# Kernel optimization log

Measured on AMD Instinct MI355X. Metric: run time of the kernel, lower is better.

## Reference

```python
import jax, jax.numpy as jnp
import numpy as np

N_LOC = 20000
N_EXP = 200000
H = 64
E = 1500000
L = 400000


def setup_inputs() -> dict:
    key = jax.random.key(0)
    ks = jax.random.split(key, 24)
    f = jnp.float32
    w = lambda k, shp: jax.random.normal(k, shp, dtype=f) * 0.1
    # edges: ('location','of','experts'): src in [0,N_LOC), dst in [0,N_EXP)
    src = jax.random.randint(ks[0], (E,), 0, N_LOC)
    dst = jax.random.randint(ks[1], (E,), 0, N_EXP)
    edge_of = jnp.stack([src, dst])          # location -> experts
    edge_rev = jnp.stack([dst, src])         # experts -> location (ToUndirected)
    row = jax.random.randint(ks[2], (L,), 0, N_LOC)
    col = jax.random.randint(ks[3], (L,), 0, N_EXP)
    edge_label_index = jnp.stack([row, col])
    return dict(
        emb_loc=w(ks[4], (N_LOC, H)), emb_exp=w(ks[5], (N_EXP, H)),
        W1l_of=w(ks[6], (H, H)), b1_of=jnp.zeros((H,), f), W1r_of=w(ks[7], (H, H)),
        W1l_rev=w(ks[8], (H, H)), b1_rev=jnp.zeros((H,), f), W1r_rev=w(ks[9], (H, H)),
        W2l_of=w(ks[10], (H, H)), b2_of=jnp.zeros((H,), f), W2r_of=w(ks[11], (H, H)),
        W2l_rev=w(ks[12], (H, H)), b2_rev=jnp.zeros((H,), f), W2r_rev=w(ks[13], (H, H)),
        dW1=w(ks[14], (2 * H, H)), db1=jnp.zeros((H,), f),
        dW2=w(ks[15], (H, 1)), db2=jnp.zeros((1,), f),
        edge_of=edge_of, edge_rev=edge_rev, edge_label_index=edge_label_index,
    )


def _sage(x_src, x_dst, edge, Wl, b, Wr, n_dst):
    # PyG SAGEConv: lin_l(mean of neighbor msgs) + lin_r(x_dst); bias only in lin_l
    s, d = edge[0], edge[1]
    msg = x_src[s]                                   # [E, H] gather
    summed = jax.ops.segment_sum(msg, d, num_segments=n_dst)
    cnt = jax.ops.segment_sum(jnp.ones((edge.shape[1],), x_src.dtype), d, num_segments=n_dst)
    agg = summed / jnp.maximum(cnt, 1.0)[:, None]
    return agg @ Wl + b + x_dst @ Wr


def reference(emb_loc, emb_exp,
              W1l_of, b1_of, W1r_of, W1l_rev, b1_rev, W1r_rev,
              W2l_of, b2_of, W2r_of, W2l_rev, b2_rev, W2r_rev,
              dW1, db1, dW2, db2,
              edge_of, edge_rev, edge_label_index):
    # layer 1 (to_hetero: one conv per edge type; each dst type has one incoming type)
    z_exp = jax.nn.relu(_sage(emb_loc, emb_exp, edge_of, W1l_of, b1_of, W1r_of, N_EXP))
    z_loc = jax.nn.relu(_sage(emb_exp, emb_loc, edge_rev, W1l_rev, b1_rev, W1r_rev, N_LOC))
    # layer 2 (no relu)
    z_exp2 = _sage(z_loc, z_exp, edge_of, W2l_of, b2_of, W2r_of, N_EXP)
    z_loc2 = _sage(z_exp, z_loc, edge_rev, W2l_rev, b2_rev, W2r_rev, N_LOC)
    # EdgeDecoder: gather-concat-MLP
    row, col = edge_label_index[0], edge_label_index[1]
    z = jnp.concatenate([z_loc2[row], z_exp2[col]], axis=-1)  # [L, 2H]
    h = jax.nn.relu(z @ dW1 + db1)
    out = (h @ dW2 + db2).reshape(-1)
    return out
```

## Files before the change

kernel.cpp:

```cpp
#include <hip/hip_runtime.h>

#define H 64
#define NE 1500000
#define NLOC 20000
#define NEXP 200000
#define NL 400000
#define PAD_E 32
#define PAD_L 128

#define EB 896
#define NBE 224
#define LB 112
#define NBL 179
#define BIN_CHUNK 2048
#define NBIN ((NE + BIN_CHUNK - 1) / BIN_CHUNK)
#define EBSLOT 28
#define LBSLOT 32
#define ECAP 8192
#define LCAP 10240
#define FCAP 4096

#define WS_NEED 90546112ULL

typedef int vint4 __attribute__((ext_vector_type(4)));
typedef _Float16 f16x8 __attribute__((ext_vector_type(8)));
typedef _Float16 f16x4 __attribute__((ext_vector_type(4)));
typedef float f32x4 __attribute__((ext_vector_type(4)));
typedef unsigned int u32;
typedef unsigned short u16;
typedef unsigned long long u64;

__device__ __forceinline__ float bcastf(float v, int k) {
  return __int_as_float(__builtin_amdgcn_readlane(__float_as_int(v), k));
}
__device__ __forceinline__ int bcasti(int v, int k) {
  return __builtin_amdgcn_readlane(v, k);
}
__device__ __forceinline__ int sel4(int g, int n0, int n1, int n2, int n3) {
  return (g & 2) ? ((g & 1) ? n3 : n2) : ((g & 1) ? n1 : n0);
}

__global__ __launch_bounds__(256) void bin_kernel(
    const int* __restrict__ src, const int* __restrict__ dst,
    u32* __restrict__ expQ, u32* __restrict__ locQ,
    int* __restrict__ qcnt, int* __restrict__ flbk_cnt,
    u64* __restrict__ flbkQ)
{
  __shared__ u32 eb[NBE * EBSLOT];
  __shared__ u32 lb[NBL * LBSLOT];
  __shared__ int ec[NBE], lc[NBL], ebase[NBE], lbase[NBL];

  const int tid = threadIdx.x;
  for (int i = tid; i < NBE; i += 256) ec[i] = 0;
  for (int i = tid; i < NBL; i += 256) lc[i] = 0;
  __syncthreads();

  const long base = (long)blockIdx.x * BIN_CHUNK + tid * 8;
  if (base < NE) {
    vint4 s0 = __builtin_nontemporal_load((const vint4*)(src + base));
    vint4 s1 = __builtin_nontemporal_load((const vint4*)(src + base + 4));
    vint4 d0 = __builtin_nontemporal_load((const vint4*)(dst + base));
    vint4 d1 = __builtin_nontemporal_load((const vint4*)(dst + base + 4));
    int ss[8] = {s0.x, s0.y, s0.z, s0.w, s1.x, s1.y, s1.z, s1.w};
    int dd[8] = {d0.x, d0.y, d0.z, d0.w, d1.x, d1.y, d1.z, d1.w};
#pragma unroll
    for (int k = 0; k < 8; k++) {
      const u32 d = (u32)dd[k], s = (u32)ss[k];
      {
        const u32 b = d / (u32)EB;
        const int pos = atomicAdd(&ec[b], 1);
        if (pos < EBSLOT) {
          eb[b * EBSLOT + pos] = ((d - b * EB) << 16) | s;
        } else {
          int fi = atomicAdd(flbk_cnt, 1);
          if (fi < FCAP) flbkQ[fi] = ((u64)d << 32) | (u64)s;
        }
      }
      {
        const u32 b = s / (u32)LB;
        const int pos = atomicAdd(&lc[b], 1);
        if (pos < LBSLOT) {
          lb[b * LBSLOT + pos] = ((s - b * LB) << 18) | d;
        } else {
          int fi = atomicAdd(flbk_cnt, 1);
          if (fi < FCAP) flbkQ[fi] = (1ULL << 63) | ((u64)s << 32) | (u64)d;
        }
      }
    }
  }
  __syncthreads();

  for (int i = tid; i < NBE; i += 256) {
    const int c = min(ec[i], EBSLOT);
    ebase[i] = c ? atomicAdd(&qcnt[i], c) : 0;
  }
  for (int i = tid; i < NBL; i += 256) {
    const int c = min(lc[i], LBSLOT);
    lbase[i] = c ? atomicAdd(&qcnt[NBE + i], c) : 0;
  }
  __syncthreads();

  const int wid = tid >> 6, ln = tid & 63;
  for (int b = wid; b < NBE; b += 4) {
    const int c = min(ec[b], EBSLOT);
    if (ln < c) {
      const int idx = ebase[b] + ln;
      const u32 r = eb[b * EBSLOT + ln];
      if (idx < ECAP) {
        expQ[(long)b * ECAP + idx] = r;
      } else {
        int fi = atomicAdd(flbk_cnt, 1);
        if (fi < FCAP)
          flbkQ[fi] = ((u64)(b * EB + (r >> 16)) << 32) | (u64)(r & 0xFFFF);
      }
    }
  }
  for (int b = wid; b < NBL; b += 4) {
    const int c = min(lc[b], LBSLOT);
    if (ln < c) {
      const int idx = lbase[b] + ln;
      const u32 r = lb[b * LBSLOT + ln];
      if (idx < LCAP) {
        locQ[(long)b * LCAP + idx] = r;
      } else {
        int fi = atomicAdd(flbk_cnt, 1);
        if (fi < FCAP)
          flbkQ[fi] = (1ULL << 63) | ((u64)(b * LB + (r >> 18)) << 32) |
                      (u64)(r & 0x3FFFF);
      }
    }
  }
}

__global__ __launch_bounds__(256) void build_kernel(
    const u32* __restrict__ expQ, const u32* __restrict__ locQ,
    const int* __restrict__ qcnt,
    u16* __restrict__ nbr_exp, int* __restrict__ nbr_loc,
    int* __restrict__ cnt_exp, int* __restrict__ cnt_loc)
{
  __shared__ char ldsraw[60928];
  const int tid = threadIdx.x;
  if (blockIdx.x < NBE) {
    const int b = blockIdx.x;
    u16* rows = (u16*)ldsraw;
    int* cnts = (int*)(ldsraw + 57344);
    for (int i = tid; i < EB; i += 256) cnts[i] = 0;
    __syncthreads();
    const int n = min(qcnt[b], ECAP);
    for (int i = tid; i < n; i += 256) {
      const u32 r = expQ[(long)b * ECAP + i];
      const int nl = (int)(r >> 16);
      const int pos = atomicAdd(&cnts[nl], 1);
      if (pos < PAD_E) rows[nl * PAD_E + pos] = (u16)(r & 0xFFFF);
    }
    __syncthreads();
    const int node0 = b * EB;
    const int nn = min(EB, NEXP - node0);
    u32* grows = (u32*)(nbr_exp + (long)node0 * PAD_E);
    const u32* lrows = (const u32*)rows;
    for (int j = tid; j < nn * (PAD_E / 2); j += 256) grows[j] = lrows[j];
    for (int i = tid; i < nn; i += 256) cnt_exp[node0 + i] = cnts[i];
  } else {
    const int b = blockIdx.x - NBE;
    int* rows = (int*)ldsraw;
    int* cnts = (int*)(ldsraw + 57344);
    for (int i = tid; i < LB; i += 256) cnts[i] = 0;
    __syncthreads();
    const int n = min(qcnt[NBE + b], LCAP);
    for (int i = tid; i < n; i += 256) {
      const u32 r = locQ[(long)b * LCAP + i];
      const int sl = (int)(r >> 18);
      const int pos = atomicAdd(&cnts[sl], 1);
      if (pos < PAD_L) rows[sl * PAD_L + pos] = (int)(r & 0x3FFFF);
    }
    __syncthreads();
    const int node0 = b * LB;
    const int nn = min(LB, NLOC - node0);
    int* grows = nbr_loc + (long)node0 * PAD_L;
    for (int j = tid; j < nn * PAD_L; j += 256) grows[j] = rows[j];
    for (int i = tid; i < nn; i += 256) cnt_loc[node0 + i] = cnts[i];
  }
}

__global__ __launch_bounds__(256) void prep_kernel(
    const float* __restrict__ W2r_of, const float* __restrict__ W2l_of,
    const float* __restrict__ W2l_rev, const float* __restrict__ W2r_rev,
    const float* __restrict__ dW1, const float* __restrict__ b2_of,
    const float* __restrict__ b2_rev,
    float* __restrict__ Wf_q, float* __restrict__ Wf_y2,
    float* __restrict__ Wf_t2, float* __restrict__ Wf_p,
    float* __restrict__ bf_q, float* __restrict__ bf_p,
    const int* __restrict__ flbk_cnt, const u64* __restrict__ flbkQ,
    u16* __restrict__ nbr_exp, int* __restrict__ nbr_loc,
    int* __restrict__ cnt_exp, int* __restrict__ cnt_loc,
    const float* __restrict__ emb_loc, _Float16* __restrict__ Ylh,
    const float* __restrict__ W1l_of,
    const float* __restrict__ W1r_of, const float* __restrict__ W1l_rev,
    const float* __restrict__ W1r_rev,
    _Float16* __restrict__ W1rT16, _Float16* __restrict__ W1lrT16,
    _Float16* __restrict__ WfqT16,
    _Float16* __restrict__ W1rRevH16, _Float16* __restrict__ Wt2H16,
    _Float16* __restrict__ WpH16)
{
  const int lane = threadIdx.x & 63;
  const int w = threadIdx.x >> 6;
  const float* dW1a = dW1;
  const float* dW1b = dW1 + H * H;
  if (blockIdx.x < 4) {
    const float* A; const float* B; float* C;
    _Float16* CT; _Float16* CH;
    switch (blockIdx.x) {
      case 0:  A = W2r_of;  B = dW1b; C = Wf_q;  CT = WfqT16; CH = nullptr; break;
      case 1:  A = W2l_of;  B = dW1b; C = Wf_y2; CT = nullptr; CH = nullptr; break;
      case 2:  A = W2l_rev; B = dW1a; C = Wf_t2; CT = nullptr; CH = Wt2H16; break;
      default: A = W2r_rev; B = dW1a; C = Wf_p;  CT = nullptr; CH = WpH16;  break;
    }
    float b[H];
#pragma unroll
    for (int k = 0; k < H; k++) b[k] = B[k * H + lane];
    for (int r = w * 16; r < w * 16 + 16; r++) {
      const float xv = A[r * H + lane];
      float a0 = 0.f, a1 = 0.f;
#pragma unroll
      for (int k = 0; k < H; k += 2) {
        a0 += bcastf(xv, k)     * b[k];
        a1 += bcastf(xv, k + 1) * b[k + 1];
      }
      const float val = a0 + a1;
      C[r * H + lane] = val;
      if (CT) CT[(long)lane * H + r] = (_Float16)val;
      if (CH) CH[(long)r * H + lane] = (_Float16)val;
    }
  } else if (blockIdx.x == 4) {
    if (w < 2) {
      const float* bv_src = (w == 0) ? b2_of : b2_rev;
      const float* B      = (w == 0) ? dW1b  : dW1a;
      float* o            = (w == 0) ? bf_q  : bf_p;
      float wk[H];
#pragma unroll
      for (int k = 0; k < H; k++) wk[k] = B[k * H + lane];
      const float bv = bv_src[lane];
      float a = 0.f;
#pragma unroll
      for (int k = 0; k < H; k++) a += bcastf(bv, k) * wk[k];
      o[lane] = a;
    }
  } else if (blockIdx.x == 5) {
    const int n = min(*flbk_cnt, FCAP);
    for (int i = threadIdx.x; i < n; i += 256) {
      const u64 rec = flbkQ[i];
      const int node = (int)((rec >> 32) & 0x3FFFF);
      const int val  = (int)(rec & 0x3FFFF);
      if ((rec >> 63) == 0) {
        int pos = atomicAdd(&cnt_exp[node], 1);
        if (pos < PAD_E) nbr_exp[(long)node * PAD_E + pos] = (u16)val;
      } else {
        int pos = atomicAdd(&cnt_loc[node], 1);
        if (pos < PAD_L) nbr_loc[(long)node * PAD_L + pos] = val;
      }
    }
  } else if (blockIdx.x < 8) {
    const float* S = (blockIdx.x == 6) ? W1r_of : W1l_rev;
    _Float16* D    = (blockIdx.x == 6) ? W1rT16 : W1lrT16;
    for (int k = w * 16; k < w * 16 + 16; k++)
      D[(long)lane * H + k] = (_Float16)S[(long)k * H + lane];
  } else if (blockIdx.x == 8) {
    for (int k = w * 16; k < w * 16 + 16; k++)
      W1rRevH16[(long)k * H + lane] = (_Float16)W1r_rev[(long)k * H + lane];
  } else {
    float wreg[H];
#pragma unroll
    for (int k = 0; k < H; k++) wreg[k] = W1l_of[k * H + lane];
    const int gw2 = (blockIdx.x - 9) * 4 + w;
    for (int r = gw2; r < NLOC; r += 5000) {
      const float xv = emb_loc[(long)r * H + lane];
      float a0 = 0.f, a1 = 0.f;
#pragma unroll
      for (int k = 0; k < H; k += 2) {
        a0 += bcastf(xv, k)     * wreg[k];
        a1 += bcastf(xv, k + 1) * wreg[k + 1];
      }
      Ylh[(long)r * H + lane] = (_Float16)(a0 + a1);
    }
  }
}

__global__ __launch_bounds__(256, 4) void dense_linear_kernel(
    const float* __restrict__ x, _Float16* __restrict__ out16,
    const float* __restrict__ W, int n)
{
  const int lane = threadIdx.x & 63;
  const int gw = (blockIdx.x * 256 + threadIdx.x) >> 6;
  const int nw = (gridDim.x * 256) >> 6;
  float w[H];
#pragma unroll
  for (int k = 0; k < H; k++) w[k] = W[k * H + lane];
  for (int i = gw; i < n; i += nw) {
    const float xv = x[i * H + lane];
    float a0 = 0.f, a1 = 0.f;
#pragma unroll
    for (int k = 0; k < H; k += 2) {
      a0 += bcastf(xv, k)     * w[k];
      a1 += bcastf(xv, k + 1) * w[k + 1];
    }
    out16[i * H + lane] = (_Float16)(a0 + a1);
  }
}

__global__ __launch_bounds__(256, 4) void mfma_pass_kernel(
    const u16* __restrict__ nbr, const int* __restrict__ cnt,
    const _Float16* __restrict__ y,
    const float* a32, const _Float16* a16,
    _Float16* out1, const _Float16* __restrict__ W1T,
    const float* __restrict__ bias, int relu,
    _Float16* out2, const _Float16* __restrict__ W2T)
{
  const int w = threadIdx.x >> 6;
  const int lane = threadIdx.x & 63;
  const int q = lane >> 4;
  const int cidx = lane & 15;
  const int rb = blockIdx.x * 16;

  __shared__ float Gs[16 * 68];

  const _Float16* bt1 = W1T + (long)(w * 16 + cidx) * H;
  f16x8 b1lo = *(const f16x8*)(bt1 + q * 8);
  f16x8 b1hi = *(const f16x8*)(bt1 + 32 + q * 8);
  f16x8 b2lo, b2hi;
  if (out2) {
    const _Float16* bt2 = W2T + (long)(w * 16 + cidx) * H;
    b2lo = *(const f16x8*)(bt2 + q * 8);
    b2hi = *(const f16x8*)(bt2 + 32 + q * 8);
  }

  f16x8 a0, a1;
  if (a16) {
    const _Float16* ar = a16 + (long)(rb + cidx) * H;
    a0 = *(const f16x8*)(ar + q * 8);
    a1 = *(const f16x8*)(ar + 32 + q * 8);
  } else {
    const float* ar = a32 + (long)(rb + cidx) * H;
    f32x4 v0 = *(const f32x4*)(ar + q * 8);
    f32x4 v1 = *(const f32x4*)(ar + q * 8 + 4);
    f32x4 v2 = *(const f32x4*)(ar + 32 + q * 8);
    f32x4 v3 = *(const f32x4*)(ar + 32 + q * 8 + 4);
#pragma unroll
    for (int j = 0; j < 4; j++) {
      a0[j] = (_Float16)v0[j];
      a0[j + 4] = (_Float16)v1[j];
      a1[j] = (_Float16)v2[j];
      a1[j + 4] = (_Float16)v3[j];
    }
  }

  if (y) {
    const int i0r = rb + w * 4;
    const int g = lane >> 4;
    const int sub = lane & 15;
    int c4v[4];
#pragma unroll
    for (int rr = 0; rr < 4; rr++) c4v[rr] = cnt[i0r + rr];
    int id4[4];
#pragma unroll
    for (int rr = 0; rr < 4; rr++) {
      const int c = min(c4v[rr], PAD_E);
      id4[rr] = (lane < c) ? (int)nbr[(long)(i0r + rr) * PAD_E + lane] : 0;
    }
#pragma unroll
    for (int rr = 0; rr < 4; rr++) {
      const int cc = min(c4v[rr], PAD_E);
      const int id = id4[rr];
      const int kl = cc - 1;
      float s0 = 0.f, s1 = 0.f, s2 = 0.f, s3 = 0.f;
      for (int k = 0; k < cc; k += 4) {
        const int n0 = bcasti(id, k);
        const int n1 = bcasti(id, min(k + 1, kl));
        const int n2 = bcasti(id, min(k + 2, kl));
        const int n3 = bcasti(id, min(k + 3, kl));
        const int ns = sel4(g, n0, n1, n2, n3);
        const f16x4 v = *(const f16x4*)(y + (long)ns * H + sub * 4);
        const float msk = (k + g < cc) ? 1.0f : 0.0f;
        s0 = fmaf(msk, (float)v[0], s0);
        s1 = fmaf(msk, (float)v[1], s1);
        s2 = fmaf(msk, (float)v[2], s2);
        s3 = fmaf(msk, (float)v[3], s3);
      }
      s0 += __shfl_xor(s0, 16); s0 += __shfl_xor(s0, 32);
      s1 += __shfl_xor(s1, 16); s1 += __shfl_xor(s1, 32);
      s2 += __shfl_xor(s2, 16); s2 += __shfl_xor(s2, 32);
      s3 += __shfl_xor(s3, 16); s3 += __shfl_xor(s3, 32);
      const float inv = 1.0f / fmaxf((float)c4v[rr], 1.0f);
      if (lane < 16) {
        float* gp = &Gs[(w * 4 + rr) * 68 + 4 * lane];
        gp[0] = s0 * inv; gp[1] = s1 * inv;
        gp[2] = s2 * inv; gp[3] = s3 * inv;
      }
    }
  }

  f32x4 acc1 = {0.f, 0.f, 0.f, 0.f};
  acc1 = __builtin_amdgcn_mfma_f32_16x16x32_f16(a0, b1lo, acc1, 0, 0, 0);
  acc1 = __builtin_amdgcn_mfma_f32_16x16x32_f16(a1, b1hi, acc1, 0, 0, 0);
  f32x4 acc2 = {0.f, 0.f, 0.f, 0.f};
  if (out2) {
    acc2 = __builtin_amdgcn_mfma_f32_16x16x32_f16(a0, b2lo, acc2, 0, 0, 0);
    acc2 = __builtin_amdgcn_mfma_f32_16x16x32_f16(a1, b2hi, acc2, 0, 0, 0);
  }

  const float bj = bias ? bias[w * 16 + cidx] : 0.f;
  __syncthreads();
#pragma unroll
  for (int reg = 0; reg < 4; reg++) {
    const int r = q * 4 + reg;
    float v = acc1[reg] + bj;
    if (y) v += Gs[r * 68 + w * 16 + cidx];
    if (relu) v = fmaxf(v, 0.f);
    out1[(long)(rb + r) * H + w * 16 + cidx] = (_Float16)v;
    if (out2)
      out2[(long)(rb + r) * H + w * 16 + cidx] = (_Float16)acc2[reg];
  }
}

__global__ __launch_bounds__(256, 6) void loc_z_kernel(
    const int* __restrict__ nbr, const int* __restrict__ cnt,
    const _Float16* __restrict__ T1, const float* __restrict__ x,
    float* __restrict__ z_out,
    const _Float16* __restrict__ Wr16, const float* __restrict__ b1)
{
  __shared__ _Float16 Wl[4096];
  const int tid = threadIdx.x;
  for (int j = tid * 8; j < 4096; j += 2048)
    *(f16x8*)&Wl[j] = *(const f16x8*)&Wr16[j];
  __syncthreads();

  const int lane = tid & 63;
  const int gw = (blockIdx.x * 256 + tid) >> 6;
  const int nw = (gridDim.x * 256) >> 6;
  const int g = lane >> 4;
  const int sub = lane & 15;
  const float bj = b1[lane];
  for (int i = gw; i < NLOC; i += nw) {
    const int c = cnt[i];
    const int cc = min(c, PAD_L);
    const int* nb = nbr + (long)i * PAD_L;
    float t0 = 0.f, t1 = 0.f, t2 = 0.f, t3 = 0.f;
    int e = 0;
    while (e < cc) {
      const int m = min(cc - e, 64);
      const int id = (lane < m) ? nb[e + lane] : 0;
      const int ml = m - 1;
      for (int k = 0; k < m; k += 4) {
        const int n0 = bcasti(id, k);
        const int n1 = bcasti(id, min(k + 1, ml));
        const int n2 = bcasti(id, min(k + 2, ml));
        const int n3 = bcasti(id, min(k + 3, ml));
        const int ns = sel4(g, n0, n1, n2, n3);
        const f16x4 v = *(const f16x4*)(T1 + (long)ns * H + sub * 4);
        const float mk = (k + g < m) ? 1.0f : 0.0f;
        t0 = fmaf(mk, (float)v[0], t0);
        t1 = fmaf(mk, (float)v[1], t1);
        t2 = fmaf(mk, (float)v[2], t2);
        t3 = fmaf(mk, (float)v[3], t3);
      }
      e += m;
    }
    t0 += __shfl_xor(t0, 16); t0 += __shfl_xor(t0, 32);
    t1 += __shfl_xor(t1, 16); t1 += __shfl_xor(t1, 32);
    t2 += __shfl_xor(t2, 16); t2 += __shfl_xor(t2, 32);
    t3 += __shfl_xor(t3, 16); t3 += __shfl_xor(t3, 32);
    const int srcl = lane >> 2;
    const int r2 = lane & 3;
    const float vt0 = __shfl(t0, srcl), vt1 = __shfl(t1, srcl);
    const float vt2 = __shfl(t2, srcl), vt3 = __shfl(t3, srcl);
    const float g1 = ((r2 & 2) ? ((r2 & 1) ? vt3 : vt2)
                               : ((r2 & 1) ? vt1 : vt0)) /
                     fmaxf((float)c, 1.0f);
    const float xv = x[(long)i * H + lane];
    float a0 = 0.f, a1 = 0.f;
#pragma unroll
    for (int k = 0; k < H; k += 2) {
      a0 = fmaf(bcastf(xv, k),     (float)Wl[k * H + lane], a0);
      a1 = fmaf(bcastf(xv, k + 1), (float)Wl[(k + 1) * H + lane], a1);
    }
    z_out[(long)i * H + lane] = fmaxf(g1 + bj + a0 + a1, 0.0f);
  }
}

__global__ __launch_bounds__(256, 6) void loc_ph_kernel(
    const int* __restrict__ nbr, const int* __restrict__ cnt,
    const _Float16* __restrict__ ZEt, const float* __restrict__ z_loc,
    _Float16* __restrict__ ph_out,
    const _Float16* __restrict__ Wt216, const _Float16* __restrict__ Wp16,
    const float* __restrict__ bfp)
{
  __shared__ _Float16 Wl[2 * 4096];
  const int tid = threadIdx.x;
  for (int j = tid * 8; j < 4096; j += 2048) {
    *(f16x8*)&Wl[j]        = *(const f16x8*)&Wt216[j];
    *(f16x8*)&Wl[4096 + j] = *(const f16x8*)&Wp16[j];
  }
  __syncthreads();

  const int lane = tid & 63;
  const int gw = (blockIdx.x * 256 + tid) >> 6;
  const int nw = (gridDim.x * 256) >> 6;
  const int g = lane >> 4;
  const int sub = lane & 15;
  const float bp = bfp[lane];
  for (int i = gw; i < NLOC; i += nw) {
    const int c = cnt[i];
    const int cc = min(c, PAD_L);
    const int* nb = nbr + (long)i * PAD_L;
    float u0 = 0.f, u1 = 0.f, u2 = 0.f, u3 = 0.f;
    int e = 0;
    while (e < cc) {
      const int m = min(cc - e, 64);
      const int id = (lane < m) ? nb[e + lane] : 0;
      const int ml = m - 1;
      for (int k = 0; k < m; k += 4) {
        const int n0 = bcasti(id, k);
        const int n1 = bcasti(id, min(k + 1, ml));
        const int n2 = bcasti(id, min(k + 2, ml));
        const int n3 = bcasti(id, min(k + 3, ml));
        const int ns = sel4(g, n0, n1, n2, n3);
        const f16x4 v = *(const f16x4*)(ZEt + (long)ns * H + sub * 4);
        const float mk = (k + g < m) ? 1.0f : 0.0f;
        u0 = fmaf(mk, (float)v[0], u0);
        u1 = fmaf(mk, (float)v[1], u1);
        u2 = fmaf(mk, (float)v[2], u2);
        u3 = fmaf(mk, (float)v[3], u3);
      }
      e += m;
    }
    u0 += __shfl_xor(u0, 16); u0 += __shfl_xor(u0, 32);
    u1 += __shfl_xor(u1, 16); u1 += __shfl_xor(u1, 32);
    u2 += __shfl_xor(u2, 16); u2 += __shfl_xor(u2, 32);
    u3 += __shfl_xor(u3, 16); u3 += __shfl_xor(u3, 32);
    const int srcl = lane >> 2;
    const int r2 = lane & 3;
    const float vu0 = __shfl(u0, srcl), vu1 = __shfl(u1, srcl);
    const float vu2 = __shfl(u2, srcl), vu3 = __shfl(u3, srcl);
    const float gz = ((r2 & 2) ? ((r2 & 1) ? vu3 : vu2)
                               : ((r2 & 1) ? vu1 : vu0)) /
                     fmaxf((float)c, 1.0f);
    const float zv = z_loc[(long)i * H + lane];
    float p0 = 0.f, p1 = 0.f;
#pragma unroll
    for (int k = 0; k < H; k += 2) {
      p0 = fmaf(bcastf(gz, k),     (float)Wl[k * H + lane], p0);
      p0 = fmaf(bcastf(zv, k),     (float)Wl[4096 + k * H + lane], p0);
      p1 = fmaf(bcastf(gz, k + 1), (float)Wl[(k + 1) * H + lane], p1);
      p1 = fmaf(bcastf(zv, k + 1), (float)Wl[4096 + (k + 1) * H + lane], p1);
    }
    ph_out[(long)i * H + lane] = (_Float16)(p0 + p1 + bp);
  }
}

__global__ __launch_bounds__(256, 4) void edge_kernel(
    const int* __restrict__ row, const int* __restrict__ col,
    const _Float16* __restrict__ P, const _Float16* __restrict__ Q,
    const float* __restrict__ db1, const float* __restrict__ dW2,
    const float* __restrict__ db2, float* __restrict__ out)
{
  const int lane = threadIdx.x & 63;
  const int gw = (blockIdx.x * 256 + threadIdx.x) >> 6;
  const int nw = (gridDim.x * 256) >> 6;
  const int g = lane >> 4;
  const int sub = lane & 15;
  const f32x4 bj4 = *(const f32x4*)(db1 + 4 * sub);
  const f32x4 w24 = *(const f32x4*)(dW2 + 4 * sub);
  const float b2 = db2[0];
  for (int e = gw * 4; e < NL; e += nw * 4) {
    const int r0 = row[e], r1 = row[e + 1], r2i = row[e + 2], r3 = row[e + 3];
    const int c0 = col[e], c1 = col[e + 1], c2i = col[e + 2], c3 = col[e + 3];
    const int rs = sel4(g, r0, r1, r2i, r3);
    const int cs = sel4(g, c0, c1, c2i, c3);
    const f16x4 pv = *(const f16x4*)(P + (long)rs * H + sub * 4);
    const f16x4 qv = *(const f16x4*)(Q + (long)cs * H + sub * 4);
    float h = fmaxf((float)pv[0] + (float)qv[0] + bj4[0], 0.f) * w24[0]
            + fmaxf((float)pv[1] + (float)qv[1] + bj4[1], 0.f) * w24[1]
            + fmaxf((float)pv[2] + (float)qv[2] + bj4[2], 0.f) * w24[2]
            + fmaxf((float)pv[3] + (float)qv[3] + bj4[3], 0.f) * w24[3];
    h += __shfl_xor(h, 1);
    h += __shfl_xor(h, 2);
    h += __shfl_xor(h, 4);
    h += __shfl_xor(h, 8);
    if (sub == 0) out[e + g] = h + b2;
  }
}

extern "C" void kernel_launch(void* const* d_in, const int* in_sizes, int n_in,
                              void* d_out, int out_size, void* d_ws, size_t ws_size,
                              hipStream_t stream) {
  const float* emb_loc = (const float*)d_in[0];
  const float* emb_exp = (const float*)d_in[1];
  const float* W1l_of  = (const float*)d_in[2];
  const float* b1_of   = (const float*)d_in[3];
  const float* W1r_of  = (const float*)d_in[4];
  const float* W1l_rev = (const float*)d_in[5];
  const float* b1_rev  = (const float*)d_in[6];
  const float* W1r_rev = (const float*)d_in[7];
  const float* W2l_of  = (const float*)d_in[8];
  const float* b2_of   = (const float*)d_in[9];
  const float* W2r_of  = (const float*)d_in[10];
  const float* W2l_rev = (const float*)d_in[11];
  const float* b2_rev  = (const float*)d_in[12];
  const float* W2r_rev = (const float*)d_in[13];
  const float* dW1     = (const float*)d_in[14];
  const float* db1     = (const float*)d_in[15];
  const float* dW2     = (const float*)d_in[16];
  const float* db2     = (const float*)d_in[17];
  const int*   edge_of = (const int*)d_in[18];
  const int*   eli     = (const int*)d_in[20];

  const int* src = edge_of;
  const int* dst = edge_of + NE;
  const int* row = eli;
  const int* col = eli + NL;

  if (ws_size < WS_NEED) return;

  char* ws = (char*)d_ws;
  int*            cnt_loc = (int*)(ws);
  int*            cnt_exp = (int*)(ws + 80000);
  int*            nbr_loc = (int*)(ws + 880064);
  unsigned short* nbr_exp = (unsigned short*)(ws + 11120064);
  _Float16*       Ylh     = (_Float16*)(ws + 23920064);
  _Float16*       Y2fh    = (_Float16*)(ws + 26480064);
  float*          z_loc   = (float*)(ws + 29040064);
  _Float16*       PH      = (_Float16*)(ws + 34160064);
  _Float16*       W1rT16  = (_Float16*)(ws + 36720064);
  _Float16*       W1lrT16 = (_Float16*)(ws + 36728256);
  _Float16*       WfqT16  = (_Float16*)(ws + 36736448);
  _Float16*       W1rRevH16 = (_Float16*)(ws + 36752832);
  _Float16*       Wt2H16  = (_Float16*)(ws + 36761024);
  _Float16*       WpH16   = (_Float16*)(ws + 36769216);
  _Float16*       ZE      = (_Float16*)(ws + 39280064);
  _Float16*       TH      = (_Float16*)(ws + 64880064);
  u32*            expQ    = (u32*)(ws + 64880064);
  u32*            locQ    = (u32*)(ws + 72220096);
  int*            qcnt    = (int*)(ws + 79551936);
  int*            flbk    = (int*)(ws + 79553552);
  u64*            flbkQ   = (u64*)(ws + 79554048);
  float*          Wf_q    = (float*)(ws + 90480064);
  float*          Wf_y2   = (float*)(ws + 90496448);
  float*          Wf_t2   = (float*)(ws + 90512832);
  float*          Wf_p    = (float*)(ws + 90529216);
  float*          bf_q    = (float*)(ws + 90545600);
  float*          bf_p    = (float*)(ws + 90545856);
  float*          out     = (float*)d_out;

  (void)hipMemsetAsync(ws + 79551936, 0, 2048, stream);

  bin_kernel<<<NBIN, 256, 0, stream>>>(src, dst, expQ, locQ, qcnt, flbk, flbkQ);
  build_kernel<<<NBE + NBL, 256, 0, stream>>>(expQ, locQ, qcnt,
      nbr_exp, nbr_loc, cnt_exp, cnt_loc);
  prep_kernel<<<1259, 256, 0, stream>>>(W2r_of, W2l_of, W2l_rev, W2r_rev,
                                        dW1, b2_of, b2_rev,
                                        Wf_q, Wf_y2, Wf_t2, Wf_p, bf_q, bf_p,
                                        flbk, flbkQ, nbr_exp, nbr_loc,
                                        cnt_exp, cnt_loc,
                                        emb_loc, Ylh, W1l_of,
                                        W1r_of, W1l_rev, W1r_rev,
                                        W1rT16, W1lrT16, WfqT16,
                                        W1rRevH16, Wt2H16, WpH16);

  mfma_pass_kernel<<<NEXP / 16, 256, 0, stream>>>(nbr_exp, cnt_exp, Ylh,
      emb_exp, (const _Float16*)nullptr, ZE, W1rT16, b1_of, 1, TH, W1lrT16);
  loc_z_kernel<<<1536, 256, 0, stream>>>(nbr_loc, cnt_loc, TH,
      emb_loc, z_loc, W1rRevH16, b1_rev);
  loc_ph_kernel<<<1536, 256, 0, stream>>>(nbr_loc, cnt_loc, ZE,
      z_loc, PH, Wt2H16, WpH16, bf_p);
  dense_linear_kernel<<<1280, 256, 0, stream>>>(z_loc, Y2fh, Wf_y2, NLOC);
  mfma_pass_kernel<<<NEXP / 16, 256, 0, stream>>>(nbr_exp, cnt_exp, Y2fh,
      (const float*)nullptr, ZE, ZE, WfqT16, bf_q, 0,
      (_Float16*)nullptr, (const _Float16*)nullptr);
  edge_kernel<<<2048, 256, 0, stream>>>(row, col, PH, ZE,
                                        db1, dW2, db2, out);
}
```

Before: 584.8 us.

## Process four location nodes per wave with sorted neighbor lists in gathers

Each location neighbor list is padded with a sentinel and bitonic-sorted in the build kernel. The loc_z and loc_ph kernels now give each wave four nodes, one per 16-lane group, and run a fixed 128-step gather loop that samples each node's neighbors proportionally. This replaces the old per-node sequential loop, which left three quarters of the lanes idle on reductions, and the sorted indices should improve locality of the gathered rows. In exchange it always does 128 steps regardless of degree, with masked redundant loads for low-degree nodes, and adds sorting cost to the build.

```diff
diff --git a/kernel.cpp b/kernel.cpp
--- a/kernel.cpp
+++ b/kernel.cpp
@@ -38,6 +38,9 @@
 }
 __device__ __forceinline__ int sel4(int g, int n0, int n1, int n2, int n3) {
   return (g & 2) ? ((g & 1) ? n3 : n2) : ((g & 1) ? n1 : n0);
+}
+__device__ __forceinline__ float sel4f(int g, float a, float b, float c, float d) {
+  return (g & 2) ? ((g & 1) ? d : c) : ((g & 1) ? b : a);
 }
 
 __global__ __launch_bounds__(256) void bin_kernel(
@@ -165,6 +168,7 @@
     int* rows = (int*)ldsraw;
     int* cnts = (int*)(ldsraw + 57344);
     for (int i = tid; i < LB; i += 256) cnts[i] = 0;
+    for (int i = tid; i < LB * PAD_L; i += 256) rows[i] = 0x3FFFF;
     __syncthreads();
     const int n = min(qcnt[NBE + b], LCAP);
     for (int i = tid; i < n; i += 256) {
@@ -172,6 +176,29 @@
       const int sl = (int)(r >> 18);
       const int pos = atomicAdd(&cnts[sl], 1);
       if (pos < PAD_L) rows[sl * PAD_L + pos] = (int)(r & 0x3FFFF);
+    }
+    __syncthreads();
+    const int ln = tid & 63, wd = tid >> 6;
+    for (int r = wd; r < LB; r += 4) {
+      int* row = rows + r * PAD_L;
+      int v0 = row[ln], v1 = row[64 + ln];
+      for (int k = 2; k <= 128; k <<= 1) {
+        for (int j = k >> 1; j >= 1; j >>= 1) {
+          if (j == 64) {
+            const int a = min(v0, v1), bmx = max(v0, v1);
+            v0 = a; v1 = bmx;
+          } else {
+            const int p0 = __shfl_xor(v0, j);
+            const int p1 = __shfl_xor(v1, j);
+            const bool up = ((ln & j) == 0);
+            const bool a0 = ((ln & k) == 0);
+            const bool a1 = (((ln + 64) & k) == 0);
+            v0 = (up == a0) ? min(v0, p0) : max(v0, p0);
+            v1 = (up == a1) ? min(v1, p1) : max(v1, p1);
+          }
+        }
+      }
+      row[ln] = v0; row[64 + ln] = v1;
     }
     __syncthreads();
     const int node0 = b * LB;
@@ -435,54 +462,59 @@
 
   const int lane = tid & 63;
   const int gw = (blockIdx.x * 256 + tid) >> 6;
-  const int nw = (gridDim.x * 256) >> 6;
-  const int g = lane >> 4;
-  const int sub = lane & 15;
+  const int g = lane >> 4, sub = lane & 15;
+  const int base = gw * 4;
   const float bj = b1[lane];
-  for (int i = gw; i < NLOC; i += nw) {
-    const int c = cnt[i];
-    const int cc = min(c, PAD_L);
-    const int* nb = nbr + (long)i * PAD_L;
-    float t0 = 0.f, t1 = 0.f, t2 = 0.f, t3 = 0.f;
-    int e = 0;
-    while (e < cc) {
-      const int m = min(cc - e, 64);
-      const int id = (lane < m) ? nb[e + lane] : 0;
-      const int ml = m - 1;
-      for (int k = 0; k < m; k += 4) {
-        const int n0 = bcasti(id, k);
-        const int n1 = bcasti(id, min(k + 1, ml));
-        const int n2 = bcasti(id, min(k + 2, ml));
-        const int n3 = bcasti(id, min(k + 3, ml));
-        const int ns = sel4(g, n0, n1, n2, n3);
-        const f16x4 v = *(const f16x4*)(T1 + (long)ns * H + sub * 4);
-        const float mk = (k + g < m) ? 1.0f : 0.0f;
-        t0 = fmaf(mk, (float)v[0], t0);
-        t1 = fmaf(mk, (float)v[1], t1);
-        t2 = fmaf(mk, (float)v[2], t2);
-        t3 = fmaf(mk, (float)v[3], t3);
-      }
-      e += m;
-    }
-    t0 += __shfl_xor(t0, 16); t0 += __shfl_xor(t0, 32);
-    t1 += __shfl_xor(t1, 16); t1 += __shfl_xor(t1, 32);
-    t2 += __shfl_xor(t2, 16); t2 += __shfl_xor(t2, 32);
-    t3 += __shfl_xor(t3, 16); t3 += __shfl_xor(t3, 32);
-    const int srcl = lane >> 2;
-    const int r2 = lane & 3;
-    const float vt0 = __shfl(t0, srcl), vt1 = __shfl(t1, srcl);
-    const float vt2 = __shfl(t2, srcl), vt3 = __shfl(t3, srcl);
-    const float g1 = ((r2 & 2) ? ((r2 & 1) ? vt3 : vt2)
-                               : ((r2 & 1) ? vt1 : vt0)) /
-                     fmaxf((float)c, 1.0f);
-    const float xv = x[(long)i * H + lane];
+
+  int cf[4], cc[4];
+#pragma unroll
+  for (int r = 0; r < 4; r++) { cf[r] = cnt[base + r]; cc[r] = min(cf[r], PAD_L); }
+  int idA[4], idB[4];
+#pragma unroll
+  for (int r = 0; r < 4; r++) {
+    const int* nb = nbr + (long)(base + r) * PAD_L;
+    idA[r] = min(nb[lane], NEXP - 1);
+    idB[r] = min(nb[64 + lane], NEXP - 1);
+  }
+
+  float s0 = 0.f, s1 = 0.f, s2 = 0.f, s3 = 0.f;
+  int idx[4] = {0, 0, 0, 0};
+  for (int p = 0; p < 128; p++) {
+    int e[4]; float mk[4];
+#pragma unroll
+    for (int r = 0; r < 4; r++) {
+      const int ni = (p * cc[r]) >> 7;
+      const bool val = (p == 0) ? (cc[r] > 0) : (ni != idx[r]);
+      idx[r] = ni;
+      const int lo = bcasti(idA[r], ni & 63);
+      const int hi = bcasti(idB[r], ni & 63);
+      e[r] = (ni < 64) ? lo : hi;
+      mk[r] = val ? 1.0f : 0.0f;
+    }
+    const int es = sel4(g, e[0], e[1], e[2], e[3]);
+    const float ms = sel4f(g, mk[0], mk[1], mk[2], mk[3]);
+    const f16x4 v = *(const f16x4*)(T1 + (long)es * H + sub * 4);
+    s0 = fmaf(ms, (float)v[0], s0);
+    s1 = fmaf(ms, (float)v[1], s1);
+    s2 = fmaf(ms, (float)v[2], s2);
+    s3 = fmaf(ms, (float)v[3], s3);
+  }
+
+#pragma unroll
+  for (int r = 0; r < 4; r++) {
+    const int srcl = r * 16 + (lane >> 2);
+    const float w0 = __shfl(s0, srcl), w1 = __shfl(s1, srcl);
+    const float w2v = __shfl(s2, srcl), w3 = __shfl(s3, srcl);
+    const float agg = sel4f(lane & 3, w0, w1, w2v, w3) /
+                      fmaxf((float)cf[r], 1.0f);
+    const float xv = x[(long)(base + r) * H + lane];
     float a0 = 0.f, a1 = 0.f;
 #pragma unroll
     for (int k = 0; k < H; k += 2) {
       a0 = fmaf(bcastf(xv, k),     (float)Wl[k * H + lane], a0);
       a1 = fmaf(bcastf(xv, k + 1), (float)Wl[(k + 1) * H + lane], a1);
     }
-    z_out[(long)i * H + lane] = fmaxf(g1 + bj + a0 + a1, 0.0f);
+    z_out[(long)(base + r) * H + lane] = fmaxf(agg + bj + a0 + a1, 0.0f);
   }
 }
 
@@ -503,47 +535,52 @@
 
   const int lane = tid & 63;
   const int gw = (blockIdx.x * 256 + tid) >> 6;
-  const int nw = (gridDim.x * 256) >> 6;
-  const int g = lane >> 4;
-  const int sub = lane & 15;
+  const int g = lane >> 4, sub = lane & 15;
+  const int base = gw * 4;
   const float bp = bfp[lane];
-  for (int i = gw; i < NLOC; i += nw) {
-    const int c = cnt[i];
-    const int cc = min(c, PAD_L);
-    const int* nb = nbr + (long)i * PAD_L;
-    float u0 = 0.f, u1 = 0.f, u2 = 0.f, u3 = 0.f;
-    int e = 0;
-    while (e < cc) {
-      const int m = min(cc - e, 64);
-      const int id = (lane < m) ? nb[e + lane] : 0;
-      const int ml = m - 1;
-      for (int k = 0; k < m; k += 4) {
-        const int n0 = bcasti(id, k);
-        const int n1 = bcasti(id, min(k + 1, ml));
-        const int n2 = bcasti(id, min(k + 2, ml));
-        const int n3 = bcasti(id, min(k + 3, ml));
-        const int ns = sel4(g, n0, n1, n2, n3);
-        const f16x4 v = *(const f16x4*)(ZEt + (long)ns * H + sub * 4);
-        const float mk = (k + g < m) ? 1.0f : 0.0f;
-        u0 = fmaf(mk, (float)v[0], u0);
-        u1 = fmaf(mk, (float)v[1], u1);
-        u2 = fmaf(mk, (float)v[2], u2);
-        u3 = fmaf(mk, (float)v[3], u3);
-      }
-      e += m;
-    }
-    u0 += __shfl_xor(u0, 16); u0 += __shfl_xor(u0, 32);
-    u1 += __shfl_xor(u1, 16); u1 += __shfl_xor(u1, 32);
-    u2 += __shfl_xor(u2, 16); u2 += __shfl_xor(u2, 32);
-    u3 += __shfl_xor(u3, 16); u3 += __shfl_xor(u3, 32);
-    const int srcl = lane >> 2;
-    const int r2 = lane & 3;
-    const float vu0 = __shfl(u0, srcl), vu1 = __shfl(u1, srcl);
-    const float vu2 = __shfl(u2, srcl), vu3 = __shfl(u3, srcl);
-    const float gz = ((r2 & 2) ? ((r2 & 1) ? vu3 : vu2)
-                               : ((r2 & 1) ? vu1 : vu0)) /
-                     fmaxf((float)c, 1.0f);
-    const float zv = z_loc[(long)i * H + lane];
+
+  int cf[4], cc[4];
+#pragma unroll
+  for (int r = 0; r < 4; r++) { cf[r] = cnt[base + r]; cc[r] = min(cf[r], PAD_L); }
+  int idA[4], idB[4];
+#pragma unroll
+  for (int r = 0; r < 4; r++) {
+    const int* nb = nbr + (long)(base + r) * PAD_L;
+    idA[r] = min(nb[lane], NEXP - 1);
+    idB[r] = min(nb[64 + lane], NEXP - 1);
+  }
+
+  float s0 = 0.f, s1 = 0.f, s2 = 0.f, s3 = 0.f;
+  int idx[4] = {0, 0, 0, 0};
+  for (int p = 0; p < 128; p++) {
+    int e[4]; float mk[4];
+#pragma unroll
+    for (int r = 0; r < 4; r++) {
+      const int ni = (p * cc[r]) >> 7;
+      const bool val = (p == 0) ? (cc[r] > 0) : (ni != idx[r]);
+      idx[r] = ni;
+      const int lo = bcasti(idA[r], ni & 63);
+      const int hi = bcasti(idB[r], ni & 63);
+      e[r] = (ni < 64) ? lo : hi;
+      mk[r] = val ? 1.0f : 0.0f;
+    }
+    const int es = sel4(g, e[0], e[1], e[2], e[3]);
+    const float ms = sel4f(g, mk[0], mk[1], mk[2], mk[3]);
+    const f16x4 v = *(const f16x4*)(ZEt + (long)es * H + sub * 4);
+    s0 = fmaf(ms, (float)v[0], s0);
+    s1 = fmaf(ms, (float)v[1], s1);
+    s2 = fmaf(ms, (float)v[2], s2);
+    s3 = fmaf(ms, (float)v[3], s3);
+  }
+
+#pragma unroll
+  for (int r = 0; r < 4; r++) {
+    const int srcl = r * 16 + (lane >> 2);
+    const float w0 = __shfl(s0, srcl), w1 = __shfl(s1, srcl);
+    const float w2v = __shfl(s2, srcl), w3 = __shfl(s3, srcl);
+    const float gz = sel4f(lane & 3, w0, w1, w2v, w3) /
+                     fmaxf((float)cf[r], 1.0f);
+    const float zv = z_loc[(long)(base + r) * H + lane];
     float p0 = 0.f, p1 = 0.f;
 #pragma unroll
     for (int k = 0; k < H; k += 2) {
@@ -552,7 +589,7 @@
       p1 = fmaf(bcastf(gz, k + 1), (float)Wl[(k + 1) * H + lane], p1);
       p1 = fmaf(bcastf(zv, k + 1), (float)Wl[4096 + (k + 1) * H + lane], p1);
     }
-    ph_out[(long)i * H + lane] = (_Float16)(p0 + p1 + bp);
+    ph_out[(long)(base + r) * H + lane] = (_Float16)(p0 + p1 + bp);
   }
 }
 
@@ -667,9 +704,9 @@
 
   mfma_pass_kernel<<<NEXP / 16, 256, 0, stream>>>(nbr_exp, cnt_exp, Ylh,
       emb_exp, (const _Float16*)nullptr, ZE, W1rT16, b1_of, 1, TH, W1lrT16);
-  loc_z_kernel<<<1536, 256, 0, stream>>>(nbr_loc, cnt_loc, TH,
+  loc_z_kernel<<<1250, 256, 0, stream>>>(nbr_loc, cnt_loc, TH,
       emb_loc, z_loc, W1rRevH16, b1_rev);
-  loc_ph_kernel<<<1536, 256, 0, stream>>>(nbr_loc, cnt_loc, ZE,
+  loc_ph_kernel<<<1250, 256, 0, stream>>>(nbr_loc, cnt_loc, ZE,
       z_loc, PH, Wt2H16, WpH16, bf_p);
   dense_linear_kernel<<<1280, 256, 0, stream>>>(z_loc, Y2fh, Wf_y2, NLOC);
   mfma_pass_kernel<<<NEXP / 16, 256, 0, stream>>>(nbr_exp, cnt_exp, Y2fh,
```

After: 610.8 us. +4.5%, slower.

## Sort location neighbor lists and switch loc gathers to lane-per-feature loads

Applied to the files above, without the earlier changes.

Location neighbor lists are now bitonic-sorted in the build kernel, padded with a sentinel, so gathers visit source rows in ascending order for better cache locality. Both location gather kernels drop the 4-group f16x4 gather with cross-lane reductions and instead read one half per lane per neighbor, with 8 independent accumulators. The first location kernel now keeps the fp32 W1r_rev weights in registers instead of an fp16 LDS copy, which removes one prep block. Grids grow to 2048 blocks and occupancy hints drop to 4, trading the extra sort work and lower occupancy for more loads in flight.

```diff
diff --git a/kernel.cpp b/kernel.cpp
--- a/kernel.cpp
+++ b/kernel.cpp
@@ -165,6 +165,7 @@
     int* rows = (int*)ldsraw;
     int* cnts = (int*)(ldsraw + 57344);
     for (int i = tid; i < LB; i += 256) cnts[i] = 0;
+    for (int i = tid; i < LB * PAD_L; i += 256) rows[i] = 0x3FFFF;
     __syncthreads();
     const int n = min(qcnt[NBE + b], LCAP);
     for (int i = tid; i < n; i += 256) {
@@ -172,6 +173,29 @@
       const int sl = (int)(r >> 18);
       const int pos = atomicAdd(&cnts[sl], 1);
       if (pos < PAD_L) rows[sl * PAD_L + pos] = (int)(r & 0x3FFFF);
+    }
+    __syncthreads();
+    const int ln = tid & 63, wd = tid >> 6;
+    for (int r = wd; r < LB; r += 4) {
+      int* row = rows + r * PAD_L;
+      int v0 = row[ln], v1 = row[64 + ln];
+      for (int k = 2; k <= 128; k <<= 1) {
+        for (int j = k >> 1; j >= 1; j >>= 1) {
+          if (j == 64) {
+            const int a = min(v0, v1), bmx = max(v0, v1);
+            v0 = a; v1 = bmx;
+          } else {
+            const int p0 = __shfl_xor(v0, j);
+            const int p1 = __shfl_xor(v1, j);
+            const bool up = ((ln & j) == 0);
+            const bool a0 = ((ln & k) == 0);
+            const bool a1 = (((ln + 64) & k) == 0);
+            v0 = (up == a0) ? min(v0, p0) : max(v0, p0);
+            v1 = (up == a1) ? min(v1, p1) : max(v1, p1);
+          }
+        }
+      }
+      row[ln] = v0; row[64 + ln] = v1;
     }
     __syncthreads();
     const int node0 = b * LB;
@@ -196,11 +220,9 @@
     const float* __restrict__ emb_loc, _Float16* __restrict__ Ylh,
     const float* __restrict__ W1l_of,
     const float* __restrict__ W1r_of, const float* __restrict__ W1l_rev,
-    const float* __restrict__ W1r_rev,
     _Float16* __restrict__ W1rT16, _Float16* __restrict__ W1lrT16,
     _Float16* __restrict__ WfqT16,
-    _Float16* __restrict__ W1rRevH16, _Float16* __restrict__ Wt2H16,
-    _Float16* __restrict__ WpH16)
+    _Float16* __restrict__ Wt2H16, _Float16* __restrict__ WpH16)
 {
   const int lane = threadIdx.x & 63;
   const int w = threadIdx.x >> 6;
@@ -264,14 +286,11 @@
     _Float16* D    = (blockIdx.x == 6) ? W1rT16 : W1lrT16;
     for (int k = w * 16; k < w * 16 + 16; k++)
       D[(long)lane * H + k] = (_Float16)S[(long)k * H + lane];
-  } else if (blockIdx.x == 8) {
-    for (int k = w * 16; k < w * 16 + 16; k++)
-      W1rRevH16[(long)k * H + lane] = (_Float16)W1r_rev[(long)k * H + lane];
   } else {
     float wreg[H];
 #pragma unroll
     for (int k = 0; k < H; k++) wreg[k] = W1l_of[k * H + lane];
-    const int gw2 = (blockIdx.x - 9) * 4 + w;
+    const int gw2 = (blockIdx.x - 8) * 4 + w;
     for (int r = gw2; r < NLOC; r += 5000) {
       const float xv = emb_loc[(long)r * H + lane];
       float a0 = 0.f, a1 = 0.f;
@@ -421,72 +440,74 @@
   }
 }
 
-__global__ __launch_bounds__(256, 6) void loc_z_kernel(
+__global__ __launch_bounds__(256, 4) void loc_gather_kernel(
     const int* __restrict__ nbr, const int* __restrict__ cnt,
-    const _Float16* __restrict__ T1, const float* __restrict__ x,
-    float* __restrict__ z_out,
-    const _Float16* __restrict__ Wr16, const float* __restrict__ b1)
+    const _Float16* __restrict__ T, const float* __restrict__ x,
+    float* __restrict__ out32,
+    const float* __restrict__ Wr, const float* __restrict__ bias,
+    int n, int relu)
 {
-  __shared__ _Float16 Wl[4096];
-  const int tid = threadIdx.x;
-  for (int j = tid * 8; j < 4096; j += 2048)
-    *(f16x8*)&Wl[j] = *(const f16x8*)&Wr16[j];
-  __syncthreads();
-
-  const int lane = tid & 63;
-  const int gw = (blockIdx.x * 256 + tid) >> 6;
+  const int lane = threadIdx.x & 63;
+  const int gw = (blockIdx.x * 256 + threadIdx.x) >> 6;
   const int nw = (gridDim.x * 256) >> 6;
-  const int g = lane >> 4;
-  const int sub = lane & 15;
-  const float bj = b1[lane];
-  for (int i = gw; i < NLOC; i += nw) {
+  float wr[H];
+#pragma unroll
+  for (int k = 0; k < H; k++) wr[k] = Wr[k * H + lane];
+  const float bj = bias[lane];
+  for (int i = gw; i < n; i += nw) {
     const int c = cnt[i];
     const int cc = min(c, PAD_L);
     const int* nb = nbr + (long)i * PAD_L;
-    float t0 = 0.f, t1 = 0.f, t2 = 0.f, t3 = 0.f;
+    float s0 = 0.f, s1 = 0.f, s2 = 0.f, s3 = 0.f;
+    float s4 = 0.f, s5 = 0.f, s6 = 0.f, s7 = 0.f;
     int e = 0;
     while (e < cc) {
       const int m = min(cc - e, 64);
       const int id = (lane < m) ? nb[e + lane] : 0;
-      const int ml = m - 1;
-      for (int k = 0; k < m; k += 4) {
-        const int n0 = bcasti(id, k);
-        const int n1 = bcasti(id, min(k + 1, ml));
-        const int n2 = bcasti(id, min(k + 2, ml));
-        const int n3 = bcasti(id, min(k + 3, ml));
-        const int ns = sel4(g, n0, n1, n2, n3);
-        const f16x4 v = *(const f16x4*)(T1 + (long)ns * H + sub * 4);
-        const float mk = (k + g < m) ? 1.0f : 0.0f;
-        t0 = fmaf(mk, (float)v[0], t0);
-        t1 = fmaf(mk, (float)v[1], t1);
-        t2 = fmaf(mk, (float)v[2], t2);
-        t3 = fmaf(mk, (float)v[3], t3);
-      }
+      int k = 0;
+      const int m8 = m & ~7;
+      for (; k < m8; k += 8) {
+        const int i0 = bcasti(id, k),     i1 = bcasti(id, k + 1),
+                  i2 = bcasti(id, k + 2), i3 = bcasti(id, k + 3),
+                  i4 = bcasti(id, k + 4), i5 = bcasti(id, k + 5),
+                  i6 = bcasti(id, k + 6), i7 = bcasti(id, k + 7);
+        s0 += (float)T[(long)i0 * H + lane];
+        s1 += (float)T[(long)i1 * H + lane];
+        s2 += (float)T[(long)i2 * H + lane];
+        s3 += (float)T[(long)i3 * H + lane];
+        s4 += (float)T[(long)i4 * H + lane];
+        s5 += (float)T[(long)i5 * H + lane];
+        s6 += (float)T[(long)i6 * H + lane];
+        s7 += (float)T[(long)i7 * H + lane];
+      }
+      const int m4 = m & ~3;
+      for (; k < m4; k += 4) {
+        const int i0 = bcasti(id, k), i1 = bcasti(id, k + 1),
+                  i2 = bcasti(id, k + 2), i3 = bcasti(id, k + 3);
+        s0 += (float)T[(long)i0 * H + lane];
+        s1 += (float)T[(long)i1 * H + lane];
+        s2 += (float)T[(long)i2 * H + lane];
+        s3 += (float)T[(long)i3 * H + lane];
+      }
+      for (; k < m; k++) s0 += (float)T[(long)bcasti(id, k) * H + lane];
       e += m;
     }
-    t0 += __shfl_xor(t0, 16); t0 += __shfl_xor(t0, 32);
-    t1 += __shfl_xor(t1, 16); t1 += __shfl_xor(t1, 32);
-    t2 += __shfl_xor(t2, 16); t2 += __shfl_xor(t2, 32);
-    t3 += __shfl_xor(t3, 16); t3 += __shfl_xor(t3, 32);
-    const int srcl = lane >> 2;
-    const int r2 = lane & 3;
-    const float vt0 = __shfl(t0, srcl), vt1 = __shfl(t1, srcl);
-    const float vt2 = __shfl(t2, srcl), vt3 = __shfl(t3, srcl);
-    const float g1 = ((r2 & 2) ? ((r2 & 1) ? vt3 : vt2)
-                               : ((r2 & 1) ? vt1 : vt0)) /
-                     fmaxf((float)c, 1.0f);
+    const float agg = (((s0 + s1) + (s2 + s3)) + ((s4 + s5) + (s6 + s7))) /
+                      fmaxf((float)c, 1.0f);
     const float xv = x[(long)i * H + lane];
     float a0 = 0.f, a1 = 0.f;
 #pragma unroll
     for (int k = 0; k < H; k += 2) {
-      a0 = fmaf(bcastf(xv, k),     (float)Wl[k * H + lane], a0);
-      a1 = fmaf(bcastf(xv, k + 1), (float)Wl[(k + 1) * H + lane], a1);
-    }
-    z_out[(long)i * H + lane] = fmaxf(g1 + bj + a0 + a1, 0.0f);
-  }
-}
-
-__global__ __launch_bounds__(256, 6) void loc_ph_kernel(
+      a0 += bcastf(xv, k)     * wr[k];
+      a1 += bcastf(xv, k + 1) * wr[k + 1];
+    }
+    float acc = agg + bj + a0 + a1;
+    if (relu) acc = fmaxf(acc, 0.0f);
+    out32[(long)i * H + lane] = acc;
+  }
+}
+
+__global__ __launch_bounds__(256, 4) void loc_ph_kernel(
     const int* __restrict__ nbr, const int* __restrict__ cnt,
     const _Float16* __restrict__ ZEt, const float* __restrict__ z_loc,
     _Float16* __restrict__ ph_out,
@@ -504,44 +525,46 @@
   const int lane = tid & 63;
   const int gw = (blockIdx.x * 256 + tid) >> 6;
   const int nw = (gridDim.x * 256) >> 6;
-  const int g = lane >> 4;
-  const int sub = lane & 15;
   const float bp = bfp[lane];
   for (int i = gw; i < NLOC; i += nw) {
     const int c = cnt[i];
     const int cc = min(c, PAD_L);
     const int* nb = nbr + (long)i * PAD_L;
-    float u0 = 0.f, u1 = 0.f, u2 = 0.f, u3 = 0.f;
+    float s0 = 0.f, s1 = 0.f, s2 = 0.f, s3 = 0.f;
+    float s4 = 0.f, s5 = 0.f, s6 = 0.f, s7 = 0.f;
     int e = 0;
     while (e < cc) {
       const int m = min(cc - e, 64);
       const int id = (lane < m) ? nb[e + lane] : 0;
-      const int ml = m - 1;
-      for (int k = 0; k < m; k += 4) {
-        const int n0 = bcasti(id, k);
-        const int n1 = bcasti(id, min(k + 1, ml));
-        const int n2 = bcasti(id, min(k + 2, ml));
-        const int n3 = bcasti(id, min(k + 3, ml));
-        const int ns = sel4(g, n0, n1, n2, n3);
-        const f16x4 v = *(const f16x4*)(ZEt + (long)ns * H + sub * 4);
-        const float mk = (k + g < m) ? 1.0f : 0.0f;
-        u0 = fmaf(mk, (float)v[0], u0);
-        u1 = fmaf(mk, (float)v[1], u1);
-        u2 = fmaf(mk, (float)v[2], u2);
-        u3 = fmaf(mk, (float)v[3], u3);
-      }
+      int k = 0;
+      const int m8 = m & ~7;
+      for (; k < m8; k += 8) {
+        const int i0 = bcasti(id, k),     i1 = bcasti(id, k + 1),
+                  i2 = bcasti(id, k + 2), i3 = bcasti(id, k + 3),
+                  i4 = bcasti(id, k + 4), i5 = bcasti(id, k + 5),
+                  i6 = bcasti(id, k + 6), i7 = bcasti(id, k + 7);
+        s0 += (float)ZEt[(long)i0 * H + lane];
+        s1 += (float)ZEt[(long)i1 * H + lane];
+        s2 += (float)ZEt[(long)i2 * H + lane];
+        s3 += (float)ZEt[(long)i3 * H + lane];
+        s4 += (float)ZEt[(long)i4 * H + lane];
+        s5 += (float)ZEt[(long)i5 * H + lane];
+        s6 += (float)ZEt[(long)i6 * H + lane];
+        s7 += (float)ZEt[(long)i7 * H + lane];
+      }
+      const int m4 = m & ~3;
+      for (; k < m4; k += 4) {
+        const int i0 = bcasti(id, k), i1 = bcasti(id, k + 1),
+                  i2 = bcasti(id, k + 2), i3 = bcasti(id, k + 3);
+        s0 += (float)ZEt[(long)i0 * H + lane];
+        s1 += (float)ZEt[(long)i1 * H + lane];
+        s2 += (float)ZEt[(long)i2 * H + lane];
+        s3 += (float)ZEt[(long)i3 * H + lane];
+      }
+      for (; k < m; k++) s0 += (float)ZEt[(long)bcasti(id, k) * H + lane];
       e += m;
     }
-    u0 += __shfl_xor(u0, 16); u0 += __shfl_xor(u0, 32);
-    u1 += __shfl_xor(u1, 16); u1 += __shfl_xor(u1, 32);
-    u2 += __shfl_xor(u2, 16); u2 += __shfl_xor(u2, 32);
-    u3 += __shfl_xor(u3, 16); u3 += __shfl_xor(u3, 32);
-    const int srcl = lane >> 2;
-    const int r2 = lane & 3;
-    const float vu0 = __shfl(u0, srcl), vu1 = __shfl(u1, srcl);
-    const float vu2 = __shfl(u2, srcl), vu3 = __shfl(u3, srcl);
-    const float gz = ((r2 & 2) ? ((r2 & 1) ? vu3 : vu2)
-                               : ((r2 & 1) ? vu1 : vu0)) /
+    const float gz = (((s0 + s1) + (s2 + s3)) + ((s4 + s5) + (s6 + s7))) /
                      fmaxf((float)c, 1.0f);
     const float zv = z_loc[(long)i * H + lane];
     float p0 = 0.f, p1 = 0.f;
@@ -632,7 +655,6 @@
   _Float16*       W1rT16  = (_Float16*)(ws + 36720064);
   _Float16*       W1lrT16 = (_Float16*)(ws + 36728256);
   _Float16*       WfqT16  = (_Float16*)(ws + 36736448);
-  _Float16*       W1rRevH16 = (_Float16*)(ws + 36752832);
   _Float16*       Wt2H16  = (_Float16*)(ws + 36761024);
   _Float16*       WpH16   = (_Float16*)(ws + 36769216);
   _Float16*       ZE      = (_Float16*)(ws + 39280064);
@@ -655,21 +677,21 @@
   bin_kernel<<<NBIN, 256, 0, stream>>>(src, dst, expQ, locQ, qcnt, flbk, flbkQ);
   build_kernel<<<NBE + NBL, 256, 0, stream>>>(expQ, locQ, qcnt,
       nbr_exp, nbr_loc, cnt_exp, cnt_loc);
-  prep_kernel<<<1259, 256, 0, stream>>>(W2r_of, W2l_of, W2l_rev, W2r_rev,
+  prep_kernel<<<1258, 256, 0, stream>>>(W2r_of, W2l_of, W2l_rev, W2r_rev,
                                         dW1, b2_of, b2_rev,
                                         Wf_q, Wf_y2, Wf_t2, Wf_p, bf_q, bf_p,
                                         flbk, flbkQ, nbr_exp, nbr_loc,
                                         cnt_exp, cnt_loc,
                                         emb_loc, Ylh, W1l_of,
-                                        W1r_of, W1l_rev, W1r_rev,
+                                        W1r_of, W1l_rev,
                                         W1rT16, W1lrT16, WfqT16,
-                                        W1rRevH16, Wt2H16, WpH16);
+                                        Wt2H16, WpH16);
 
   mfma_pass_kernel<<<NEXP / 16, 256, 0, stream>>>(nbr_exp, cnt_exp, Ylh,
       emb_exp, (const _Float16*)nullptr, ZE, W1rT16, b1_of, 1, TH, W1lrT16);
-  loc_z_kernel<<<1536, 256, 0, stream>>>(nbr_loc, cnt_loc, TH,
-      emb_loc, z_loc, W1rRevH16, b1_rev);
-  loc_ph_kernel<<<1536, 256, 0, stream>>>(nbr_loc, cnt_loc, ZE,
+  loc_gather_kernel<<<2048, 256, 0, stream>>>(nbr_loc, cnt_loc, TH,
+      emb_loc, z_loc, W1r_rev, b1_rev, NLOC, 1);
+  loc_ph_kernel<<<2048, 256, 0, stream>>>(nbr_loc, cnt_loc, ZE,
       z_loc, PH, Wt2H16, WpH16, bf_p);
   dense_linear_kernel<<<1280, 256, 0, stream>>>(z_loc, Y2fh, Wf_y2, NLOC);
   mfma_pass_kernel<<<NEXP / 16, 256, 0, stream>>>(nbr_exp, cnt_exp, Y2fh,
```

Measured after the change: 640.6 us. 1.1x slower.
